# Kernel optimization log

Measured on AMD Instinct MI355X. Metric: run time of the kernel, lower is better.

Reference implementation:

```python
import jax, jax.numpy as jnp
import numpy as np
from jax import lax

EPS = 1e-5

def _bn(x, p):
    # p: [4, C] = (gamma, beta, running_mean, running_var); x: [B,C,H,W] (eval-mode BN)
    g, b, m, v = p
    return (x - m[None, :, None, None]) * (g / jnp.sqrt(v + EPS))[None, :, None, None] + b[None, :, None, None]

def _relu6(x):
    return jnp.clip(x, 0.0, 6.0)

def _grouped_1x1(x, w):
    # x: [B, D, H, W], w: [G, D//G]; groups=G, 1 out channel per group (contiguous channel groups)
    B, D, H, W = x.shape
    G = w.shape[0]
    xr = x.reshape(B, G, D // G, H, W)
    return jnp.einsum('bgihw,gi->bghw', xr, w)

def _pool4(x, kind):
    if kind == 'max':
        return lax.reduce_window(x, -jnp.inf, lax.max, (1, 1, 4, 4), (1, 1, 4, 4), 'VALID')
    s = lax.reduce_window(x, 0.0, lax.add, (1, 1, 4, 4), (1, 1, 4, 4), 'VALID')
    return s / 16.0

def _rel_pos_index(rh):
    # Swin-style relative position index, static numpy
    coords = np.stack(np.meshgrid(np.arange(rh), np.arange(rh), indexing='ij')).reshape(2, -1)
    rel = coords[:, :, None] - coords[:, None, :]
    rel = rel.transpose(1, 2, 0).astype(np.int64)
    rel[..., 0] += rh - 1
    rel[..., 1] += rh - 1
    rel[..., 0] *= 2 * rh - 1
    return rel.sum(-1)  # [N, N]

def _upsample_bilinear_align(x, scale):
    # UpsamplingBilinear2d => align_corners=True
    B, C, H, W = x.shape
    Ho, Wo = H * scale, W * scale
    ys = jnp.linspace(0.0, H - 1.0, Ho)
    xs = jnp.linspace(0.0, W - 1.0, Wo)
    y0 = jnp.floor(ys).astype(jnp.int32); y1 = jnp.minimum(y0 + 1, H - 1); wy = (ys - y0)[None, None, :, None]
    x0 = jnp.floor(xs).astype(jnp.int32); x1 = jnp.minimum(x0 + 1, W - 1); wx = (xs - x0)[None, None, None, :]
    rows = x[:, :, y0, :] * (1.0 - wy) + x[:, :, y1, :] * wy          # [B,C,Ho,W]
    return rows[:, :, :, x0] * (1.0 - wx) + rows[:, :, :, x1] * wx    # [B,C,Ho,Wo]

def bh_attention(x, w_le, b_le, bn_le, w_max, b_max, bn_max, w_avg, b_avg, bn_avg,
                 bias_table, w_q, w_kv, w_proj, b_proj, w_out, b_out):
    D = x.shape[1]
    G = D // 4
    # q branch: 4x4 stride-4 grouped conv (groups=G, 4 in-ch per group) + BN + ReLU6
    xq = lax.conv_general_dilated(x, w_le, window_strides=(4, 4), padding='VALID',
                                  dimension_numbers=('NCHW', 'OIHW', 'NCHW'),
                                  feature_group_count=G)
    xq = _relu6(_bn(xq + b_le[None, :, None, None], bn_le))
    B, C, H, W = xq.shape
    N = H * W
    nH = 4 if C > 64 else 2
    hd = C // nH
    xq_t = xq.reshape(B, C, N).transpose(0, 2, 1)                      # [B,N,C]
    q = (xq_t @ w_q).reshape(B, N, nH, hd).transpose(0, 2, 1, 3) * (hd ** -0.5)

    def kv_branch(t, w_g, b_g, bn_g):
        t = _relu6(_bn(_grouped_1x1(t, w_g) + b_g[None, :, None, None], bn_g))
        tt = t.reshape(B, C, N).transpose(0, 2, 1)                     # [B,N,C]
        kv = (tt @ w_kv).reshape(B, N, 2, nH, hd).transpose(2, 0, 3, 1, 4)
        return kv[0], kv[1]                                            # [B,nH,N,hd]

    k1, v1 = kv_branch(_pool4(x, 'max'), w_max, b_max, bn_max)
    k2, v2 = kv_branch(_pool4(x, 'avg'), w_avg, b_avg, bn_avg)

    idx = _rel_pos_index(H)
    bias = bias_table[idx.reshape(-1)].reshape(N, N, nH).transpose(2, 0, 1)[None]  # [1,nH,N,N]

    def attend(k, v):
        attn = jax.nn.softmax(jnp.einsum('bhnd,bhmd->bhnm', q, k) + bias, axis=-1)
        o = jnp.einsum('bhnm,bhmd->bhnd', attn, v).transpose(0, 2, 1, 3).reshape(B, N, C)
        return o @ w_proj + b_proj

    x1 = attend(k1, v1).reshape(B, H, W, C).transpose(0, 3, 1, 2)
    x2 = attend(k2, v2).reshape(B, H, W, C).transpose(0, 3, 1, 2)
    out = x1 + x2
    out = jnp.einsum('bchw,oc->bohw', out, w_out) + b_out[None, :, None, None]
    return _upsample_bilinear_align(out, 4)


def setup_inputs() -> dict:
    key = jax.random.key(0)
    dim, h, B = 384, 128, 8
    C = dim // 4            # 96
    nH = 4 if C > 64 else 2
    rh = h // 4             # 32
    ks = jax.random.split(key, 12)
    bn_id = jnp.stack([jnp.ones(C), jnp.zeros(C), jnp.zeros(C), jnp.ones(C)])
    inp = {
        'x': jax.random.normal(ks[0], (B, dim, h, h), jnp.float32),
        'w_le': jax.random.normal(ks[1], (C, 4, 4, 4), jnp.float32) * 0.05,
        'b_le': jnp.zeros((C,), jnp.float32),
        'bn_le': bn_id,
        'w_max': jax.random.normal(ks[2], (C, 4), jnp.float32) * 0.1,
        'b_max': jnp.zeros((C,), jnp.float32),
        'bn_max': bn_id,
        'w_avg': jax.random.normal(ks[3], (C, 4), jnp.float32) * 0.1,
        'b_avg': jnp.zeros((C,), jnp.float32),
        'bn_avg': bn_id,
        'bias_table': jax.random.normal(ks[4], ((2 * rh - 1) ** 2, nH), jnp.float32) * 0.02,
        'w_q': jax.random.normal(ks[5], (C, C), jnp.float32) * (C ** -0.5),
        'w_kv': jax.random.normal(ks[6], (C, 2 * C), jnp.float32) * (C ** -0.5),
        'w_proj': jax.random.normal(ks[7], (C, C), jnp.float32) * (C ** -0.5),
        'b_proj': jnp.zeros((C,), jnp.float32),
        'w_out': jax.random.normal(ks[8], (dim, C), jnp.float32) * (C ** -0.5),
        'b_out': jnp.zeros((dim,), jnp.float32),
    }
    return inp


def reference(x, w_le, b_le, bn_le, w_max, b_max, bn_max, w_avg, b_avg, bn_avg,
              bias_table, w_q, w_kv, w_proj, b_proj, w_out, b_out):
    return bh_attention(x, w_le, b_le, bn_le, w_max, b_max, bn_max, w_avg, b_avg, bn_avg,
                        bias_table, w_q, w_kv, w_proj, b_proj, w_out, b_out)
```

## Files before the change

### kernel.cpp

```cpp
#include <hip/hip_runtime.h>
#include <math.h>

namespace {
constexpr int Bb  = 8;
constexpr int Dd  = 384;
constexpr int HIN = 128;
constexpr int Cc  = 96;
constexpr int Nn  = 1024;
constexpr int NH  = 4;
constexpr int HD  = 24;
}
#define BN_EPS 1e-5f
#define QSCALE 0.20412414523193154f

typedef unsigned short u16;
typedef unsigned int   u32;
typedef __attribute__((ext_vector_type(8))) short bh8;
typedef __attribute__((ext_vector_type(4))) float fx4;

#define MFMA16(a,b,c) __builtin_amdgcn_mfma_f32_16x16x32_bf16((a),(b),(c),0,0,0)

union PackU { u32 u[4]; bh8 s; };

__device__ __forceinline__ void split1(float v, u16& hi, u16& lo) {
    const u32 bv = __float_as_uint(v);
    const u32 hb = bv & 0xffff0000u;
    hi = (u16)(bv >> 16);
    const float r = v - __uint_as_float(hb);
    lo = (u16)(__float_as_uint(r) >> 16);
}
__device__ __forceinline__ void split2(float x, float y, u32& hi, u32& lo) {
    const u32 bx = __float_as_uint(x), by = __float_as_uint(y);
    const u32 hx = bx & 0xffff0000u, hy = by & 0xffff0000u;
    hi = (hx >> 16) | hy;
    const float rx = x - __uint_as_float(hx);
    const float ry = y - __uint_as_float(hy);
    lo = (__float_as_uint(rx) >> 16) | (__float_as_uint(ry) & 0xffff0000u);
}

__device__ __forceinline__ float bn_relu6(float y, const float* __restrict__ bn, int c) {
    float gam = bn[c], bet = bn[Cc + c], mu = bn[2*Cc + c], var = bn[3*Cc + c];
    float s = gam / sqrtf(var + BN_EPS);
    float r = (y - mu) * s + bet;
    return fminf(fmaxf(r, 0.0f), 6.0f);
}

__global__ __launch_bounds__(256) void stem_kernel(
    const float* __restrict__ x, const float* __restrict__ w_le,
    const float* __restrict__ b_le, const float* __restrict__ bn_le,
    const float* __restrict__ w_max, const float* __restrict__ b_max, const float* __restrict__ bn_max,
    const float* __restrict__ w_avg, const float* __restrict__ b_avg, const float* __restrict__ bn_avg,
    float* __restrict__ xq, float* __restrict__ tmx, float* __restrict__ tav)
{
    const int tid = threadIdx.x;
    const int n = blockIdx.x * 256 + tid;
    const int g = blockIdx.y;
    const int b = blockIdx.z;
    const int oh = n >> 5, ow = n & 31;

    const float* xb = x + (((size_t)b * Dd + 4*g) * HIN + 4*oh) * HIN + 4*ow;
    float conv = 0.0f, mxv = 0.0f, avv = 0.0f;
    #pragma unroll
    for (int i = 0; i < 4; ++i) {
        float cmax = -3.0e38f, csum = 0.0f;
        #pragma unroll
        for (int kh = 0; kh < 4; ++kh) {
            const float4 v = *(const float4*)(xb + ((size_t)i * HIN + kh) * HIN);
            const float* wl = w_le + (((g*4 + i)*4 + kh) * 4);
            conv = fmaf(v.x, wl[0], conv);
            conv = fmaf(v.y, wl[1], conv);
            conv = fmaf(v.z, wl[2], conv);
            conv = fmaf(v.w, wl[3], conv);
            cmax = fmaxf(cmax, fmaxf(fmaxf(v.x, v.y), fmaxf(v.z, v.w)));
            csum += (v.x + v.y) + (v.z + v.w);
        }
        mxv = fmaf(cmax, w_max[g*4 + i], mxv);
        avv = fmaf(csum * (1.0f/16.0f), w_avg[g*4 + i], avv);
    }
    const float xqv = bn_relu6(conv + b_le[g], bn_le, g);
    const float tm  = bn_relu6(mxv  + b_max[g], bn_max, g);
    const float ta  = bn_relu6(avv  + b_avg[g], bn_avg, g);
    const size_t o = ((size_t)b * Cc + g) * Nn + n;
    xq[o] = xqv; tmx[o] = tm; tav[o] = ta;
}

__global__ __launch_bounds__(256) void proj_kernel(
    const float* __restrict__ xq, const float* __restrict__ tmx, const float* __restrict__ tav,
    const float* __restrict__ w_q, const float* __restrict__ w_kv,
    u16* __restrict__ qhp, u16* __restrict__ qlp,
    u16* __restrict__ k1h, u16* __restrict__ k1l, u16* __restrict__ k2h, u16* __restrict__ k2l,
    u16* __restrict__ v1h, u16* __restrict__ v1l, u16* __restrict__ v2h, u16* __restrict__ v2l)
{
    const int tid = threadIdx.x;
    const int n0 = blockIdx.x * 32;
    const int b  = blockIdx.y;
    __shared__ float axq[32*101];
    __shared__ float amx[32*101];
    __shared__ float aav[32*101];
    __shared__ float lw[96*97];

    for (int e = tid; e < 96*32; e += 256) {
        const int c = e >> 5, j = e & 31;
        const size_t src = ((size_t)b * Cc + c) * Nn + n0 + j;
        axq[j*101 + c] = xq[src];
        amx[j*101 + c] = tmx[src];
        aav[j*101 + c] = tav[src];
    }

    const int tn = (tid & 7) * 4;
    const int tc = (tid >> 3) * 3;

    __syncthreads();
    for (int e = tid; e < 96*96; e += 256) lw[(e/96)*97 + (e%96)] = w_q[e];
    __syncthreads();
    {
        float acc[4][3] = {};
        for (int k = 0; k < 96; ++k) {
            const float w0 = lw[k*97 + tc + 0];
            const float w1 = lw[k*97 + tc + 1];
            const float w2 = lw[k*97 + tc + 2];
            #pragma unroll
            for (int i = 0; i < 4; ++i) {
                const float a = axq[(tn+i)*101 + k];
                acc[i][0] = fmaf(a, w0, acc[i][0]);
                acc[i][1] = fmaf(a, w1, acc[i][1]);
                acc[i][2] = fmaf(a, w2, acc[i][2]);
            }
        }
        #pragma unroll
        for (int j = 0; j < 3; ++j) {
            const int col = tc + j, hh = col / HD, d = col - hh*HD;
            #pragma unroll
            for (int i = 0; i < 4; ++i) {
                const int n = n0 + tn + i;
                u16 hi, lo;
                split1(acc[i][j] * QSCALE, hi, lo);
                const size_t dst = ((size_t)(b*NH + hh)*Nn + n)*32 + d;
                qhp[dst] = hi; qlp[dst] = lo;
            }
        }
    }

    __syncthreads();
    for (int e = tid; e < 96*96; e += 256) lw[(e/96)*97 + (e%96)] = w_kv[(e/96)*192 + (e%96)];
    __syncthreads();
    {
        float a1c[4][3] = {}, a2c[4][3] = {};
        for (int k = 0; k < 96; ++k) {
            const float w0 = lw[k*97 + tc + 0];
            const float w1 = lw[k*97 + tc + 1];
            const float w2 = lw[k*97 + tc + 2];
            #pragma unroll
            for (int i = 0; i < 4; ++i) {
                const float a1 = amx[(tn+i)*101 + k];
                const float a2 = aav[(tn+i)*101 + k];
                a1c[i][0] = fmaf(a1, w0, a1c[i][0]);
                a1c[i][1] = fmaf(a1, w1, a1c[i][1]);
                a1c[i][2] = fmaf(a1, w2, a1c[i][2]);
                a2c[i][0] = fmaf(a2, w0, a2c[i][0]);
                a2c[i][1] = fmaf(a2, w1, a2c[i][1]);
                a2c[i][2] = fmaf(a2, w2, a2c[i][2]);
            }
        }
        #pragma unroll
        for (int j = 0; j < 3; ++j) {
            const int col = tc + j, hh = col / HD, d = col - hh*HD;
            #pragma unroll
            for (int i = 0; i < 4; ++i) {
                const int n = n0 + tn + i;
                const int rho = (n & ~31) | ((n & 4) << 2) | ((n & 24) >> 1) | (n & 3);
                const size_t dst = ((size_t)(b*NH + hh)*Nn + rho)*32 + d;
                u16 hi, lo;
                split1(a1c[i][j], hi, lo); k1h[dst] = hi; k1l[dst] = lo;
                split1(a2c[i][j], hi, lo); k2h[dst] = hi; k2l[dst] = lo;
            }
        }
    }

    __syncthreads();
    for (int e = tid; e < 96*96; e += 256) lw[(e/96)*97 + (e%96)] = w_kv[(e/96)*192 + 96 + (e%96)];
    __syncthreads();
    {
        float a1c[4][3] = {}, a2c[4][3] = {};
        for (int k = 0; k < 96; ++k) {
            const float w0 = lw[k*97 + tc + 0];
            const float w1 = lw[k*97 + tc + 1];
            const float w2 = lw[k*97 + tc + 2];
            #pragma unroll
            for (int i = 0; i < 4; ++i) {
                const float a1 = amx[(tn+i)*101 + k];
                const float a2 = aav[(tn+i)*101 + k];
                a1c[i][0] = fmaf(a1, w0, a1c[i][0]);
                a1c[i][1] = fmaf(a1, w1, a1c[i][1]);
                a1c[i][2] = fmaf(a1, w2, a1c[i][2]);
                a2c[i][0] = fmaf(a2, w0, a2c[i][0]);
                a2c[i][1] = fmaf(a2, w1, a2c[i][1]);
                a2c[i][2] = fmaf(a2, w2, a2c[i][2]);
            }
        }
        #pragma unroll
        for (int j = 0; j < 3; ++j) {
            const int col = tc + j, hh = col / HD, d = col - hh*HD;
            #pragma unroll
            for (int i = 0; i < 4; ++i) {
                const int n = n0 + tn + i;
                const size_t dst = ((size_t)(b*NH + hh)*32 + d)*Nn + n;
                u16 hi, lo;
                split1(a1c[i][j], hi, lo); v1h[dst] = hi; v1l[dst] = lo;
                split1(a2c[i][j], hi, lo); v2h[dst] = hi; v2l[dst] = lo;
            }
        }
    }

    for (int e = tid; e < 1024; e += 256) {
        const int hh = e >> 8;
        const int nn = (e >> 3) & 31;
        const int d  = 24 + (e & 7);
        const int n  = n0 + nn;
        const size_t kd = ((size_t)(b*NH + hh)*Nn + n)*32 + d;
        qhp[kd] = 0; qlp[kd] = 0;
        k1h[kd] = 0; k1l[kd] = 0; k2h[kd] = 0; k2l[kd] = 0;
        const size_t vd = ((size_t)(b*NH + hh)*32 + d)*Nn + n;
        v1h[vd] = 0; v1l[vd] = 0; v2h[vd] = 0; v2l[vd] = 0;
    }
}

__global__ __launch_bounds__(256, 4) void attn_kernel(
    const u16* __restrict__ qhp, const u16* __restrict__ qlp,
    const u16* __restrict__ k1h, const u16* __restrict__ k1l,
    const u16* __restrict__ k2h, const u16* __restrict__ k2l,
    const u16* __restrict__ v1h, const u16* __restrict__ v1l,
    const u16* __restrict__ v2h, const u16* __restrict__ v2l,
    const float* __restrict__ bias_table, float* __restrict__ osum)
{
    const int tid = threadIdx.x;
    const int h = blockIdx.y, b = blockIdx.z;
    const int bh = b*NH + h;

    __shared__ float biasl[3969];
    __shared__ float mrg[2][64][21];

    for (int e = tid; e < 3969; e += 256) biasl[e] = bias_table[e*NH + h];
    __syncthreads();

    const int lane = tid & 63;
    const int wave = tid >> 6;
    const int qg = wave & 1;
    const int ks = wave >> 1;
    const int lg = lane >> 4;
    const int lr = lane & 15;
    const int q  = blockIdx.x*32 + qg*16 + lr;
    const int yn = q >> 5, xn = q & 31;

    const size_t qoff = ((size_t)bh*Nn + q)*32 + lg*8;
    const bh8 qfh = *(const bh8*)(qhp + qoff);
    const bh8 qfl = *(const bh8*)(qlp + qoff);

    const size_t kbase = ((size_t)bh*Nn + lr)*32 + lg*8;
    const size_t vbase = ((size_t)bh*32 + lr)*Nn + lg*8;
    const u16* kph[2] = { k1h + kbase, k2h + kbase };
    const u16* kpl[2] = { k1l + kbase, k2l + kbase };
    const u16* vph[2] = { v1h + vbase, v2h + vbase };
    const u16* vpl[2] = { v1l + vbase, v2l + vbase };

    const fx4 zero = {0.0f, 0.0f, 0.0f, 0.0f};
    fx4 oo[2][2];
    float mm[2], ll[2];

    #pragma unroll
    for (int br = 0; br < 2; ++br) {
        oo[br][0] = zero; oo[br][1] = zero;
        float m = -3.0e38f, l = 0.0f;
        const u16* kh = kph[br]; const u16* kl = kpl[br];
        const u16* vh = vph[br]; const u16* vl = vpl[br];

        for (int it = ks*8; it < ks*8 + 8; ++it) {
            const int kb = it*64;
            fx4 s[4];
            #pragma unroll
            for (int t = 0; t < 4; ++t) {
                const int ro = (kb + t*16)*32;
                const bh8 ah = *(const bh8*)(kh + ro);
                const bh8 al = *(const bh8*)(kl + ro);
                const int ym   = (kb >> 5) + (t >> 1);
                const int xmb  = (t & 1)*4 + lg*8;
                const int rowb = (yn - ym + 31)*63 + (xn + 31) - xmb;
                fx4 u;
                #pragma unroll
                for (int j = 0; j < 4; ++j) u[j] = biasl[rowb - j];
                u = MFMA16(ah, qfh, u);
                u = MFMA16(ah, qfl, u);
                u = MFMA16(al, qfh, u);
                s[t] = u;
            }

            float tmax = s[0][0];
            #pragma unroll
            for (int t = 0; t < 4; ++t)
                #pragma unroll
                for (int j = 0; j < 4; ++j)
                    if (t | j) tmax = fmaxf(tmax, s[t][j]);
            tmax = fmaxf(tmax, __shfl_xor(tmax, 16));
            tmax = fmaxf(tmax, __shfl_xor(tmax, 32));
            const float M = fmaxf(m, tmax);
            if (!__all(tmax <= m)) {
                const float c = __expf(m - M);
                l *= c;
                oo[br][0] *= c; oo[br][1] *= c;
            }
            m = M;

            #pragma unroll
            for (int ch = 0; ch < 2; ++ch) {
                const float e0 = __expf(s[2*ch  ][0] - M);
                const float e1 = __expf(s[2*ch  ][1] - M);
                const float e2 = __expf(s[2*ch  ][2] - M);
                const float e3 = __expf(s[2*ch  ][3] - M);
                const float e4 = __expf(s[2*ch+1][0] - M);
                const float e5 = __expf(s[2*ch+1][1] - M);
                const float e6 = __expf(s[2*ch+1][2] - M);
                const float e7 = __expf(s[2*ch+1][3] - M);
                l += ((e0 + e1) + (e2 + e3)) + ((e4 + e5) + (e6 + e7));
                PackU ph_, pl_;
                split2(e0, e1, ph_.u[0], pl_.u[0]);
                split2(e2, e3, ph_.u[1], pl_.u[1]);
                split2(e4, e5, ph_.u[2], pl_.u[2]);
                split2(e6, e7, ph_.u[3], pl_.u[3]);
                const int vo0 = kb + ch*32;
                #pragma unroll
                for (int dt = 0; dt < 2; ++dt) {
                    const size_t vo = (size_t)(dt*16)*Nn + vo0;
                    const bh8 wh = *(const bh8*)(vh + vo);
                    const bh8 wl = *(const bh8*)(vl + vo);
                    oo[br][dt] = MFMA16(wh, ph_.s, oo[br][dt]);
                    oo[br][dt] = MFMA16(wh, pl_.s, oo[br][dt]);
                    oo[br][dt] = MFMA16(wl, ph_.s, oo[br][dt]);
                }
            }
        }
        mm[br] = m; ll[br] = l;
    }

    if (ks == 1) {
        float* mb = &mrg[qg][lane][0];
        #pragma unroll
        for (int br = 0; br < 2; ++br) {
            mb[br*10 + 0] = mm[br];
            mb[br*10 + 1] = ll[br];
            #pragma unroll
            for (int j = 0; j < 4; ++j) {
                mb[br*10 + 2 + j] = oo[br][0][j];
                mb[br*10 + 6 + j] = oo[br][1][j];
            }
        }
    }
    __syncthreads();
    if (ks == 0) {
        const float* mb = &mrg[qg][lane][0];
        float li[2]; fx4 om[2][2];
        #pragma unroll
        for (int br = 0; br < 2; ++br) {
            const float mo  = mb[br*10 + 0];
            const float lo2 = mb[br*10 + 1];
            const float M  = fmaxf(mm[br], mo);
            const float ca = __expf(mm[br] - M);
            const float cb = __expf(mo - M);
            float lm = ll[br]*ca + lo2*cb;
            #pragma unroll
            for (int dt = 0; dt < 2; ++dt)
                #pragma unroll
                for (int j = 0; j < 4; ++j)
                    om[br][dt][j] = oo[br][dt][j]*ca + mb[br*10 + 2 + dt*4 + j]*cb;
            lm += __shfl_xor(lm, 16);
            lm += __shfl_xor(lm, 32);
            li[br] = 1.0f / lm;
        }
        float* orow = osum + ((size_t)b*Nn + q)*Cc + h*HD;
        #pragma unroll
        for (int dt = 0; dt < 2; ++dt)
            #pragma unroll
            for (int j = 0; j < 4; ++j) {
                const int d = dt*16 + lg*4 + j;
                if (d < HD) orow[d] = om[0][dt][j]*li[0] + om[1][dt][j]*li[1];
            }
    }
}

__global__ __launch_bounds__(256) void fusew_kernel(
    const float* __restrict__ w_proj, const float* __restrict__ b_proj,
    const float* __restrict__ w_out, const float* __restrict__ b_out,
    float* __restrict__ wf, float* __restrict__ bf)
{
    const int e = blockIdx.x * 256 + threadIdx.x;
    if (e < Cc * Dd) {
        const int c = e / Dd, o = e - c*Dd;
        const float* wp = w_proj + c*Cc;
        const float* wo = w_out + (size_t)o*Cc;
        float acc = 0.0f;
        for (int c2 = 0; c2 < Cc; ++c2) acc = fmaf(wp[c2], wo[c2], acc);
        wf[e] = acc;
    }
    if (e < Dd) {
        const float* wo = w_out + (size_t)e*Cc;
        float acc = 0.0f;
        for (int c = 0; c < Cc; ++c) acc = fmaf(b_proj[c], wo[c], acc);
        bf[e] = b_out[e] + 2.0f * acc;
    }
}

__global__ __launch_bounds__(256) void outgemm_kernel(
    const float* __restrict__ osum, const float* __restrict__ wf, const float* __restrict__ bf,
    float* __restrict__ outs)
{
    const int tid = threadIdx.x;
    const int n0 = blockIdx.x * 32;
    const int b  = blockIdx.y;
    __shared__ float ax[32*101];
    __shared__ float lw[96*132];
    for (int e = tid; e < 32*96; e += 256) {
        const int n = e / 96, c = e - n*96;
        ax[n*101 + c] = osum[((size_t)b*Nn + n0 + n)*Cc + c];
    }
    const int tn = (tid & 7) * 4;
    const int tj = (tid >> 3) * 4;
    for (int o0 = 0; o0 < Dd; o0 += 128) {
        __syncthreads();
        for (int e = tid; e < 96*128; e += 256) {
            const int c = e >> 7, j = e & 127;
            lw[c*132 + j] = wf[(size_t)c*Dd + o0 + j];
        }
        __syncthreads();
        float acc[4][4] = {};
        for (int c = 0; c < 96; ++c) {
            const float4 wv = *(const float4*)&lw[c*132 + tj];
            #pragma unroll
            for (int i = 0; i < 4; ++i) {
                const float a = ax[(tn+i)*101 + c];
                acc[i][0] = fmaf(a, wv.x, acc[i][0]);
                acc[i][1] = fmaf(a, wv.y, acc[i][1]);
                acc[i][2] = fmaf(a, wv.z, acc[i][2]);
                acc[i][3] = fmaf(a, wv.w, acc[i][3]);
            }
        }
        #pragma unroll
        for (int j = 0; j < 4; ++j) {
            const int o = o0 + tj + j;
            const float bb = bf[o];
            #pragma unroll
            for (int i = 0; i < 4; ++i)
                outs[((size_t)b*Dd + o)*Nn + n0 + tn + i] = acc[i][j] + bb;
        }
    }
}

__global__ __launch_bounds__(256) void upsample_kernel(
    const float* __restrict__ src, float* __restrict__ dst)
{
    const int gid = blockIdx.x * 256 + threadIdx.x;
    const int ox4 = gid & 31;
    const int oy  = (gid >> 5) & 127;
    const int bc  = gid >> 12;
    const float* s = src + (size_t)bc * 1024;
    const float sy = oy * (31.0f / 127.0f);
    const int y0 = (int)sy;
    const int y1 = min(y0 + 1, 31);
    const float wy = sy - (float)y0;
    const float* r0 = s + y0 * 32;
    const float* r1 = s + y1 * 32;
    float res[4];
    #pragma unroll
    for (int j = 0; j < 4; ++j) {
        const int ox = ox4 * 4 + j;
        const float sx = ox * (31.0f / 127.0f);
        const int x0 = (int)sx;
        const int x1 = min(x0 + 1, 31);
        const float wx = sx - (float)x0;
        const float t0 = r0[x0] * (1.0f - wx) + r0[x1] * wx;
        const float t1 = r1[x0] * (1.0f - wx) + r1[x1] * wx;
        res[j] = t0 * (1.0f - wy) + t1 * wy;
    }
    *(float4*)(dst + (size_t)gid * 4) = make_float4(res[0], res[1], res[2], res[3]);
}

extern "C" void kernel_launch(void* const* d_in, const int* in_sizes, int n_in,
                              void* d_out, int out_size, void* d_ws, size_t ws_size,
                              hipStream_t stream)
{
    const float* x      = (const float*)d_in[0];
    const float* w_le   = (const float*)d_in[1];
    const float* b_le   = (const float*)d_in[2];
    const float* bn_le  = (const float*)d_in[3];
    const float* w_max  = (const float*)d_in[4];
    const float* b_max  = (const float*)d_in[5];
    const float* bn_max = (const float*)d_in[6];
    const float* w_avg  = (const float*)d_in[7];
    const float* b_avg  = (const float*)d_in[8];
    const float* bn_avg = (const float*)d_in[9];
    const float* btab   = (const float*)d_in[10];
    const float* w_q    = (const float*)d_in[11];
    const float* w_kv   = (const float*)d_in[12];
    const float* w_proj = (const float*)d_in[13];
    const float* b_proj = (const float*)d_in[14];
    const float* w_out  = (const float*)d_in[15];
    const float* b_out  = (const float*)d_in[16];
    (void)in_sizes; (void)n_in; (void)out_size; (void)ws_size;

    float* ws = (float*)d_ws;
    const size_t T  = (size_t)Bb * Cc * Nn;
    const size_t AS = (size_t)Bb * NH * Nn * 32;

    float* xq   = ws + 0*T;
    float* tmx  = ws + 1*T;
    float* tav  = ws + 2*T;
    u16*  bb16  = (u16*)(ws + 3*T);
    u16* qh  = bb16 + 0*AS;  u16* ql  = bb16 + 1*AS;
    u16* k1h = bb16 + 2*AS;  u16* k1l = bb16 + 3*AS;
    u16* k2h = bb16 + 4*AS;  u16* k2l = bb16 + 5*AS;
    u16* v1h = bb16 + 6*AS;  u16* v1l = bb16 + 7*AS;
    u16* v2h = bb16 + 8*AS;  u16* v2l = bb16 + 9*AS;
    float* osum = (float*)(bb16 + 10*AS);
    float* wf   = osum + T;
    float* bf   = wf + (size_t)Cc*Dd;
    float* outs = ws;

    stem_kernel<<<dim3(4, 96, 8), 256, 0, stream>>>(
        x, w_le, b_le, bn_le, w_max, b_max, bn_max, w_avg, b_avg, bn_avg, xq, tmx, tav);
    proj_kernel<<<dim3(32, 8), 256, 0, stream>>>(
        xq, tmx, tav, w_q, w_kv, qh, ql, k1h, k1l, k2h, k2l, v1h, v1l, v2h, v2l);
    fusew_kernel<<<dim3(144), 256, 0, stream>>>(w_proj, b_proj, w_out, b_out, wf, bf);
    attn_kernel<<<dim3(32, 4, 8), 256, 0, stream>>>(
        qh, ql, k1h, k1l, k2h, k2l, v1h, v1l, v2h, v2l, btab, osum);
    outgemm_kernel<<<dim3(32, 8), 256, 0, stream>>>(osum, wf, bf, outs);
    upsample_kernel<<<dim3(49152), 256, 0, stream>>>(outs, (float*)d_out);
}
```

Baseline: 546.0 us.

## Split projection and output GEMMs across more blocks, fold weight prep into stem, lazy softmax rescale

The projection kernel now launches one block per (n-tile, batch, output kind) over five phases instead of doing all five GEMMs serially in one block, and the output GEMM is split over the three 128-column chunks. These launch more blocks for the small grids of 256 blocks. The fused-weight computation and a head-major transpose of the bias table move into an extra y-slice of the stem kernel, which removes one launch and gives the attention kernel contiguous bias loads. The online softmax now skips the max reduction and rescale unless a score exceeds the running max by more than 8, which cuts shuffles and exps but lets exponent arguments reach e^8.

```diff
diff --git a/kernel.cpp b/kernel.cpp
--- a/kernel.cpp
+++ b/kernel.cpp
@@ -50,9 +50,35 @@
     const float* __restrict__ b_le, const float* __restrict__ bn_le,
     const float* __restrict__ w_max, const float* __restrict__ b_max, const float* __restrict__ bn_max,
     const float* __restrict__ w_avg, const float* __restrict__ b_avg, const float* __restrict__ bn_avg,
-    float* __restrict__ xq, float* __restrict__ tmx, float* __restrict__ tav)
+    const float* __restrict__ w_proj, const float* __restrict__ b_proj,
+    const float* __restrict__ w_out, const float* __restrict__ b_out,
+    const float* __restrict__ btab,
+    float* __restrict__ xq, float* __restrict__ tmx, float* __restrict__ tav,
+    float* __restrict__ wf, float* __restrict__ bf, float* __restrict__ btr)
 {
     const int tid = threadIdx.x;
+    if (blockIdx.y == 96) {
+        const int tg = (blockIdx.z*4 + blockIdx.x)*256 + tid;
+        for (int e = tg; e < Cc*Dd; e += 8192) {
+            const int c = e / Dd, o = e - c*Dd;
+            const float* wp = w_proj + c*Cc;
+            const float* wo = w_out + (size_t)o*Cc;
+            float acc = 0.0f;
+            for (int c2 = 0; c2 < Cc; ++c2) acc = fmaf(wp[c2], wo[c2], acc);
+            wf[e] = acc;
+        }
+        if (tg < Dd) {
+            const float* wo = w_out + (size_t)tg*Cc;
+            float acc = 0.0f;
+            for (int c = 0; c < Cc; ++c) acc = fmaf(b_proj[c], wo[c], acc);
+            bf[tg] = b_out[tg] + 2.0f * acc;
+        }
+        for (int e = tg; e < 3969*NH; e += 8192) {
+            const int hh = e / 3969, i = e - hh*3969;
+            btr[e] = btab[i*NH + hh];
+        }
+        return;
+    }
     const int n = blockIdx.x * 256 + tid;
     const int g = blockIdx.y;
     const int b = blockIdx.z;
@@ -84,131 +110,76 @@
     xq[o] = xqv; tmx[o] = tm; tav[o] = ta;
 }
 
-__global__ __launch_bounds__(256) void proj_kernel(
+__global__ __launch_bounds__(256, 3) void proj_kernel(
     const float* __restrict__ xq, const float* __restrict__ tmx, const float* __restrict__ tav,
     const float* __restrict__ w_q, const float* __restrict__ w_kv,
     u16* __restrict__ qhp, u16* __restrict__ qlp,
     u16* __restrict__ k1h, u16* __restrict__ k1l, u16* __restrict__ k2h, u16* __restrict__ k2l,
     u16* __restrict__ v1h, u16* __restrict__ v1l, u16* __restrict__ v2h, u16* __restrict__ v2l)
 {
-    const int tid = threadIdx.x;
-    const int n0 = blockIdx.x * 32;
-    const int b  = blockIdx.y;
-    __shared__ float axq[32*101];
-    __shared__ float amx[32*101];
-    __shared__ float aav[32*101];
-    __shared__ float lw[96*97];
-
+    const int tid   = threadIdx.x;
+    const int n0    = blockIdx.x * 32;
+    const int b     = blockIdx.y;
+    const int phase = blockIdx.z;
+    __shared__ float A[32*97];
+    __shared__ float lw[96*96];
+
+    const float* asrc = (phase == 0) ? xq : ((phase == 1 || phase == 3) ? tmx : tav);
     for (int e = tid; e < 96*32; e += 256) {
         const int c = e >> 5, j = e & 31;
-        const size_t src = ((size_t)b * Cc + c) * Nn + n0 + j;
-        axq[j*101 + c] = xq[src];
-        amx[j*101 + c] = tmx[src];
-        aav[j*101 + c] = tav[src];
-    }
+        A[j*97 + c] = asrc[((size_t)b * Cc + c) * Nn + n0 + j];
+    }
+    const float* wsrc = (phase == 0) ? w_q : w_kv;
+    const int RS = (phase == 0) ? 96 : 192;
+    const int WO = (phase <= 2) ? 0 : 96;
+    for (int e = tid; e < 96*96; e += 256)
+        lw[e] = wsrc[(e/96)*RS + WO + (e%96)];
+    __syncthreads();
 
     const int tn = (tid & 7) * 4;
     const int tc = (tid >> 3) * 3;
 
-    __syncthreads();
-    for (int e = tid; e < 96*96; e += 256) lw[(e/96)*97 + (e%96)] = w_q[e];
-    __syncthreads();
-    {
-        float acc[4][3] = {};
-        for (int k = 0; k < 96; ++k) {
-            const float w0 = lw[k*97 + tc + 0];
-            const float w1 = lw[k*97 + tc + 1];
-            const float w2 = lw[k*97 + tc + 2];
-            #pragma unroll
-            for (int i = 0; i < 4; ++i) {
-                const float a = axq[(tn+i)*101 + k];
-                acc[i][0] = fmaf(a, w0, acc[i][0]);
-                acc[i][1] = fmaf(a, w1, acc[i][1]);
-                acc[i][2] = fmaf(a, w2, acc[i][2]);
-            }
-        }
-        #pragma unroll
-        for (int j = 0; j < 3; ++j) {
-            const int col = tc + j, hh = col / HD, d = col - hh*HD;
-            #pragma unroll
-            for (int i = 0; i < 4; ++i) {
-                const int n = n0 + tn + i;
-                u16 hi, lo;
-                split1(acc[i][j] * QSCALE, hi, lo);
-                const size_t dst = ((size_t)(b*NH + hh)*Nn + n)*32 + d;
-                qhp[dst] = hi; qlp[dst] = lo;
-            }
-        }
-    }
-
-    __syncthreads();
-    for (int e = tid; e < 96*96; e += 256) lw[(e/96)*97 + (e%96)] = w_kv[(e/96)*192 + (e%96)];
-    __syncthreads();
-    {
-        float a1c[4][3] = {}, a2c[4][3] = {};
-        for (int k = 0; k < 96; ++k) {
-            const float w0 = lw[k*97 + tc + 0];
-            const float w1 = lw[k*97 + tc + 1];
-            const float w2 = lw[k*97 + tc + 2];
-            #pragma unroll
-            for (int i = 0; i < 4; ++i) {
-                const float a1 = amx[(tn+i)*101 + k];
-                const float a2 = aav[(tn+i)*101 + k];
-                a1c[i][0] = fmaf(a1, w0, a1c[i][0]);
-                a1c[i][1] = fmaf(a1, w1, a1c[i][1]);
-                a1c[i][2] = fmaf(a1, w2, a1c[i][2]);
-                a2c[i][0] = fmaf(a2, w0, a2c[i][0]);
-                a2c[i][1] = fmaf(a2, w1, a2c[i][1]);
-                a2c[i][2] = fmaf(a2, w2, a2c[i][2]);
-            }
-        }
-        #pragma unroll
-        for (int j = 0; j < 3; ++j) {
-            const int col = tc + j, hh = col / HD, d = col - hh*HD;
-            #pragma unroll
-            for (int i = 0; i < 4; ++i) {
-                const int n = n0 + tn + i;
+    float acc[4][3] = {};
+    for (int k = 0; k < 96; ++k) {
+        const float w0 = lw[k*96 + tc + 0];
+        const float w1 = lw[k*96 + tc + 1];
+        const float w2 = lw[k*96 + tc + 2];
+        #pragma unroll
+        for (int i = 0; i < 4; ++i) {
+            const float a = A[(tn+i)*97 + k];
+            acc[i][0] = fmaf(a, w0, acc[i][0]);
+            acc[i][1] = fmaf(a, w1, acc[i][1]);
+            acc[i][2] = fmaf(a, w2, acc[i][2]);
+        }
+    }
+
+    u16* dh; u16* dl;
+    if      (phase == 0) { dh = qhp; dl = qlp; }
+    else if (phase == 1) { dh = k1h; dl = k1l; }
+    else if (phase == 2) { dh = k2h; dl = k2l; }
+    else if (phase == 3) { dh = v1h; dl = v1l; }
+    else                 { dh = v2h; dl = v2l; }
+
+    #pragma unroll
+    for (int j = 0; j < 3; ++j) {
+        const int col = tc + j, hh = col / HD, d = col - hh*HD;
+        #pragma unroll
+        for (int i = 0; i < 4; ++i) {
+            const int n = n0 + tn + i;
+            float v = acc[i][j];
+            size_t dst;
+            if (phase == 0) {
+                v *= QSCALE;
+                dst = ((size_t)(b*NH + hh)*Nn + n)*32 + d;
+            } else if (phase <= 2) {
                 const int rho = (n & ~31) | ((n & 4) << 2) | ((n & 24) >> 1) | (n & 3);
-                const size_t dst = ((size_t)(b*NH + hh)*Nn + rho)*32 + d;
-                u16 hi, lo;
-                split1(a1c[i][j], hi, lo); k1h[dst] = hi; k1l[dst] = lo;
-                split1(a2c[i][j], hi, lo); k2h[dst] = hi; k2l[dst] = lo;
-            }
-        }
-    }
-
-    __syncthreads();
-    for (int e = tid; e < 96*96; e += 256) lw[(e/96)*97 + (e%96)] = w_kv[(e/96)*192 + 96 + (e%96)];
-    __syncthreads();
-    {
-        float a1c[4][3] = {}, a2c[4][3] = {};
-        for (int k = 0; k < 96; ++k) {
-            const float w0 = lw[k*97 + tc + 0];
-            const float w1 = lw[k*97 + tc + 1];
-            const float w2 = lw[k*97 + tc + 2];
-            #pragma unroll
-            for (int i = 0; i < 4; ++i) {
-                const float a1 = amx[(tn+i)*101 + k];
-                const float a2 = aav[(tn+i)*101 + k];
-                a1c[i][0] = fmaf(a1, w0, a1c[i][0]);
-                a1c[i][1] = fmaf(a1, w1, a1c[i][1]);
-                a1c[i][2] = fmaf(a1, w2, a1c[i][2]);
-                a2c[i][0] = fmaf(a2, w0, a2c[i][0]);
-                a2c[i][1] = fmaf(a2, w1, a2c[i][1]);
-                a2c[i][2] = fmaf(a2, w2, a2c[i][2]);
-            }
-        }
-        #pragma unroll
-        for (int j = 0; j < 3; ++j) {
-            const int col = tc + j, hh = col / HD, d = col - hh*HD;
-            #pragma unroll
-            for (int i = 0; i < 4; ++i) {
-                const int n = n0 + tn + i;
-                const size_t dst = ((size_t)(b*NH + hh)*32 + d)*Nn + n;
-                u16 hi, lo;
-                split1(a1c[i][j], hi, lo); v1h[dst] = hi; v1l[dst] = lo;
-                split1(a2c[i][j], hi, lo); v2h[dst] = hi; v2l[dst] = lo;
-            }
+                dst = ((size_t)(b*NH + hh)*Nn + rho)*32 + d;
+            } else {
+                dst = ((size_t)(b*NH + hh)*32 + d)*Nn + n;
+            }
+            u16 hi, lo;
+            split1(v, hi, lo);
+            dh[dst] = hi; dl[dst] = lo;
         }
     }
 
@@ -217,11 +188,10 @@
         const int nn = (e >> 3) & 31;
         const int d  = 24 + (e & 7);
         const int n  = n0 + nn;
-        const size_t kd = ((size_t)(b*NH + hh)*Nn + n)*32 + d;
-        qhp[kd] = 0; qlp[kd] = 0;
-        k1h[kd] = 0; k1l[kd] = 0; k2h[kd] = 0; k2l[kd] = 0;
-        const size_t vd = ((size_t)(b*NH + hh)*32 + d)*Nn + n;
-        v1h[vd] = 0; v1l[vd] = 0; v2h[vd] = 0; v2l[vd] = 0;
+        const size_t dst = (phase <= 2)
+            ? ((size_t)(b*NH + hh)*Nn + n)*32 + d
+            : ((size_t)(b*NH + hh)*32 + d)*Nn + n;
+        dh[dst] = 0; dl[dst] = 0;
     }
 }
 
@@ -231,7 +201,7 @@
     const u16* __restrict__ k2h, const u16* __restrict__ k2l,
     const u16* __restrict__ v1h, const u16* __restrict__ v1l,
     const u16* __restrict__ v2h, const u16* __restrict__ v2l,
-    const float* __restrict__ bias_table, float* __restrict__ osum)
+    const float* __restrict__ btr, float* __restrict__ osum)
 {
     const int tid = threadIdx.x;
     const int h = blockIdx.y, b = blockIdx.z;
@@ -240,7 +210,7 @@
     __shared__ float biasl[3969];
     __shared__ float mrg[2][64][21];
 
-    for (int e = tid; e < 3969; e += 256) biasl[e] = bias_table[e*NH + h];
+    for (int e = tid; e < 3969; e += 256) biasl[e] = btr[h*3969 + e];
     __syncthreads();
 
     const int lane = tid & 63;
@@ -294,32 +264,32 @@
                 s[t] = u;
             }
 
-            float tmax = s[0][0];
-            #pragma unroll
-            for (int t = 0; t < 4; ++t)
-                #pragma unroll
-                for (int j = 0; j < 4; ++j)
-                    if (t | j) tmax = fmaxf(tmax, s[t][j]);
-            tmax = fmaxf(tmax, __shfl_xor(tmax, 16));
-            tmax = fmaxf(tmax, __shfl_xor(tmax, 32));
-            const float M = fmaxf(m, tmax);
-            if (!__all(tmax <= m)) {
+            float lmax = fmaxf(fmaxf(s[0][0], s[0][1]), fmaxf(s[0][2], s[0][3]));
+            #pragma unroll
+            for (int t = 1; t < 4; ++t)
+                lmax = fmaxf(lmax, fmaxf(fmaxf(s[t][0], s[t][1]), fmaxf(s[t][2], s[t][3])));
+
+            if (!__all(lmax <= m + 8.0f)) {
+                float tmax = lmax;
+                tmax = fmaxf(tmax, __shfl_xor(tmax, 16));
+                tmax = fmaxf(tmax, __shfl_xor(tmax, 32));
+                const float M = fmaxf(m, tmax);
                 const float c = __expf(m - M);
                 l *= c;
                 oo[br][0] *= c; oo[br][1] *= c;
-            }
-            m = M;
+                m = M;
+            }
 
             #pragma unroll
             for (int ch = 0; ch < 2; ++ch) {
-                const float e0 = __expf(s[2*ch  ][0] - M);
-                const float e1 = __expf(s[2*ch  ][1] - M);
-                const float e2 = __expf(s[2*ch  ][2] - M);
-                const float e3 = __expf(s[2*ch  ][3] - M);
-                const float e4 = __expf(s[2*ch+1][0] - M);
-                const float e5 = __expf(s[2*ch+1][1] - M);
-                const float e6 = __expf(s[2*ch+1][2] - M);
-                const float e7 = __expf(s[2*ch+1][3] - M);
+                const float e0 = __expf(s[2*ch  ][0] - m);
+                const float e1 = __expf(s[2*ch  ][1] - m);
+                const float e2 = __expf(s[2*ch  ][2] - m);
+                const float e3 = __expf(s[2*ch  ][3] - m);
+                const float e4 = __expf(s[2*ch+1][0] - m);
+                const float e5 = __expf(s[2*ch+1][1] - m);
+                const float e6 = __expf(s[2*ch+1][2] - m);
+                const float e7 = __expf(s[2*ch+1][3] - m);
                 l += ((e0 + e1) + (e2 + e3)) + ((e4 + e5) + (e6 + e7));
                 PackU ph_, pl_;
                 split2(e0, e1, ph_.u[0], pl_.u[0]);
@@ -386,28 +356,6 @@
     }
 }
 
-__global__ __launch_bounds__(256) void fusew_kernel(
-    const float* __restrict__ w_proj, const float* __restrict__ b_proj,
-    const float* __restrict__ w_out, const float* __restrict__ b_out,
-    float* __restrict__ wf, float* __restrict__ bf)
-{
-    const int e = blockIdx.x * 256 + threadIdx.x;
-    if (e < Cc * Dd) {
-        const int c = e / Dd, o = e - c*Dd;
-        const float* wp = w_proj + c*Cc;
-        const float* wo = w_out + (size_t)o*Cc;
-        float acc = 0.0f;
-        for (int c2 = 0; c2 < Cc; ++c2) acc = fmaf(wp[c2], wo[c2], acc);
-        wf[e] = acc;
-    }
-    if (e < Dd) {
-        const float* wo = w_out + (size_t)e*Cc;
-        float acc = 0.0f;
-        for (int c = 0; c < Cc; ++c) acc = fmaf(b_proj[c], wo[c], acc);
-        bf[e] = b_out[e] + 2.0f * acc;
-    }
-}
-
 __global__ __launch_bounds__(256) void outgemm_kernel(
     const float* __restrict__ osum, const float* __restrict__ wf, const float* __restrict__ bf,
     float* __restrict__ outs)
@@ -415,41 +363,39 @@
     const int tid = threadIdx.x;
     const int n0 = blockIdx.x * 32;
     const int b  = blockIdx.y;
-    __shared__ float ax[32*101];
-    __shared__ float lw[96*132];
+    const int o0 = blockIdx.z * 128;
+    __shared__ float ax[32*97];
+    __shared__ float lw[96*128];
     for (int e = tid; e < 32*96; e += 256) {
         const int n = e / 96, c = e - n*96;
-        ax[n*101 + c] = osum[((size_t)b*Nn + n0 + n)*Cc + c];
-    }
+        ax[n*97 + c] = osum[((size_t)b*Nn + n0 + n)*Cc + c];
+    }
+    for (int e = tid; e < 96*128; e += 256) {
+        const int c = e >> 7, j = e & 127;
+        lw[c*128 + j] = wf[(size_t)c*Dd + o0 + j];
+    }
+    __syncthreads();
     const int tn = (tid & 7) * 4;
     const int tj = (tid >> 3) * 4;
-    for (int o0 = 0; o0 < Dd; o0 += 128) {
-        __syncthreads();
-        for (int e = tid; e < 96*128; e += 256) {
-            const int c = e >> 7, j = e & 127;
-            lw[c*132 + j] = wf[(size_t)c*Dd + o0 + j];
-        }
-        __syncthreads();
-        float acc[4][4] = {};
-        for (int c = 0; c < 96; ++c) {
-            const float4 wv = *(const float4*)&lw[c*132 + tj];
-            #pragma unroll
-            for (int i = 0; i < 4; ++i) {
-                const float a = ax[(tn+i)*101 + c];
-                acc[i][0] = fmaf(a, wv.x, acc[i][0]);
-                acc[i][1] = fmaf(a, wv.y, acc[i][1]);
-                acc[i][2] = fmaf(a, wv.z, acc[i][2]);
-                acc[i][3] = fmaf(a, wv.w, acc[i][3]);
-            }
-        }
-        #pragma unroll
-        for (int j = 0; j < 4; ++j) {
-            const int o = o0 + tj + j;
-            const float bb = bf[o];
-            #pragma unroll
-            for (int i = 0; i < 4; ++i)
-                outs[((size_t)b*Dd + o)*Nn + n0 + tn + i] = acc[i][j] + bb;
-        }
+    float acc[4][4] = {};
+    for (int c = 0; c < 96; ++c) {
+        const float4 wv = *(const float4*)&lw[c*128 + tj];
+        #pragma unroll
+        for (int i = 0; i < 4; ++i) {
+            const float a = ax[(tn+i)*97 + c];
+            acc[i][0] = fmaf(a, wv.x, acc[i][0]);
+            acc[i][1] = fmaf(a, wv.y, acc[i][1]);
+            acc[i][2] = fmaf(a, wv.z, acc[i][2]);
+            acc[i][3] = fmaf(a, wv.w, acc[i][3]);
+        }
+    }
+    #pragma unroll
+    for (int j = 0; j < 4; ++j) {
+        const int o = o0 + tj + j;
+        const float bb = bf[o];
+        #pragma unroll
+        for (int i = 0; i < 4; ++i)
+            outs[((size_t)b*Dd + o)*Nn + n0 + tn + i] = acc[i][j] + bb;
     }
 }
 
@@ -521,15 +467,16 @@
     float* osum = (float*)(bb16 + 10*AS);
     float* wf   = osum + T;
     float* bf   = wf + (size_t)Cc*Dd;
+    float* btr  = bf + Dd;
     float* outs = ws;
 
-    stem_kernel<<<dim3(4, 96, 8), 256, 0, stream>>>(
-        x, w_le, b_le, bn_le, w_max, b_max, bn_max, w_avg, b_avg, bn_avg, xq, tmx, tav);
-    proj_kernel<<<dim3(32, 8), 256, 0, stream>>>(
+    stem_kernel<<<dim3(4, 97, 8), 256, 0, stream>>>(
+        x, w_le, b_le, bn_le, w_max, b_max, bn_max, w_avg, b_avg, bn_avg,
+        w_proj, b_proj, w_out, b_out, btab, xq, tmx, tav, wf, bf, btr);
+    proj_kernel<<<dim3(32, 8, 5), 256, 0, stream>>>(
         xq, tmx, tav, w_q, w_kv, qh, ql, k1h, k1l, k2h, k2l, v1h, v1l, v2h, v2l);
-    fusew_kernel<<<dim3(144), 256, 0, stream>>>(w_proj, b_proj, w_out, b_out, wf, bf);
     attn_kernel<<<dim3(32, 4, 8), 256, 0, stream>>>(
-        qh, ql, k1h, k1l, k2h, k2l, v1h, v1l, v2h, v2l, btab, osum);
-    outgemm_kernel<<<dim3(32, 8), 256, 0, stream>>>(osum, wf, bf, outs);
+        qh, ql, k1h, k1l, k2h, k2l, v1h, v1l, v2h, v2l, btr, osum);
+    outgemm_kernel<<<dim3(32, 8, 3), 256, 0, stream>>>(osum, wf, bf, outs);
     upsample_kernel<<<dim3(49152), 256, 0, stream>>>(outs, (float*)d_out);
 }
```

New measurement: 539.1 us. No clear change (-1.3%).
